# Kernel optimization log

Measured on AMD Instinct MI355X. Metric: run time of the kernel, lower is better.

The kernel has to match this reference:

```python
import jax, jax.numpy as jnp
import numpy as np

ASIZE, VSIZE, HSIZE, MSIZE = 128, 512, 512, 48


def _xavier(key, shape):
    fan_in, fan_out = shape[1], shape[0]
    limit = float(np.sqrt(6.0 / (fan_in + fan_out)))
    return jax.random.uniform(key, shape, jnp.float32, -limit, limit)


def setup_inputs() -> dict:
    key = jax.random.key(0)
    ks = jax.random.split(key, 9)
    B, T = 32, 64
    audio = jax.random.normal(ks[0], (B, T, ASIZE), jnp.float32)
    video = jax.random.normal(ks[1], (B, T, MSIZE, VSIZE), jnp.float32)
    return {
        "audio": audio,
        "video": video,
        "W_audio": _xavier(ks[2], (HSIZE, ASIZE)),
        "b_audio": jnp.zeros((HSIZE,), jnp.float32),
        "W_video": _xavier(ks[3], (HSIZE, VSIZE)),
        "b_video": jnp.zeros((HSIZE,), jnp.float32),
        "W_v": _xavier(ks[4], (MSIZE, HSIZE)),
        "W_g": _xavier(ks[5], (MSIZE, HSIZE)),
        "W_h": _xavier(ks[6], (1, MSIZE)),
    }


def reference(audio, video, W_audio, b_audio, W_video, b_video, W_v, W_g, W_h):
    B, T, N, vsize = video.shape  # N == MSIZE == 48 required by the broadcast
    V = video.reshape(B * T, N, vsize)                      # [BT, N, vsize]
    v = jax.nn.relu(jnp.einsum('bnv,hv->bnh', V, W_video) + b_video)  # [BT,N,h]
    a = jax.nn.relu(audio.reshape(-1, audio.shape[-1]) @ W_audio.T + b_audio)  # [BT,h]
    inter = a @ W_g.T                                        # [BT, m]
    # torch broadcast: [BT,N,m] + [BT,m,1] with N==m -> inter indexed by spatial pos
    content = jnp.einsum('bnh,mh->bnm', v, W_v) + inter[:, :, None]
    z = jnp.einsum('bnm,om->bno', jnp.tanh(content), W_h)[..., 0]  # [BT, N]
    alpha = jax.nn.softmax(z, axis=-1)                        # [BT, N]
    c = jnp.einsum('bn,bnv->bv', alpha, V)                    # [BT, vsize]
    return c.reshape(B, T, vsize)
```

## Files before the change

### kernel.cpp

```cpp
#include <hip/hip_runtime.h>
#include <hip/hip_bf16.h>

typedef __bf16 bf16x8 __attribute__((ext_vector_type(8)));
typedef __bf16 bf16x4 __attribute__((ext_vector_type(4)));
typedef float  f32x4  __attribute__((ext_vector_type(4)));

#define BT    2048
#define MDIM  48

#define WS_WVID  0
#define WS_WV    (512*512*2)
#define WS_WG    (WS_WV + 48*512*2)
#define WS_INTER (WS_WG + 48*512*2)

__global__ __launch_bounds__(256) void convert_weights(
    const float* __restrict__ Wvid, const float* __restrict__ Wv,
    const float* __restrict__ Wg,
    __bf16* __restrict__ wvid_k, __bf16* __restrict__ wv_b,
    __bf16* __restrict__ wg_b) {
    int i = blockIdx.x * blockDim.x + threadIdx.x;
    const int nv = 65536, n2 = 6144;
    if (i < nv) {
        int h = i >> 7, k4 = i & 127;
        float4 f = ((const float4*)Wvid)[i];
        bf16x4 o = {(__bf16)f.x, (__bf16)f.y, (__bf16)f.z, (__bf16)f.w};
        *(bf16x4*)(wvid_k + (size_t)(((k4 >> 1) * 512 + h) * 8 + (k4 & 1) * 4)) = o;
    } else if (i < nv + n2) {
        int j = i - nv;
        float4 f = ((const float4*)Wv)[j];
        bf16x4 o = {(__bf16)f.x, (__bf16)f.y, (__bf16)f.z, (__bf16)f.w};
        ((bf16x4*)wv_b)[j] = o;
    } else {
        int j = i - nv - n2;
        float4 f = ((const float4*)Wg)[j];
        bf16x4 o = {(__bf16)f.x, (__bf16)f.y, (__bf16)f.z, (__bf16)f.w};
        ((bf16x4*)wg_b)[j] = o;
    }
}

__global__ __launch_bounds__(512) void audio_batch(
    const float* __restrict__ audio, const float* __restrict__ Wa,
    const float* __restrict__ ba, const __bf16* __restrict__ wg_b,
    float* __restrict__ inter) {
    __shared__ float  ain[16 * 128];
    __shared__ __bf16 as_s[64 * 17 * 8];

    const int bt0 = blockIdx.x * 16;
    const int t   = threadIdx.x;

    ((float4*)ain)[t] = ((const float4*)(audio + (size_t)bt0 * 128))[t];
    __syncthreads();

    float acc[16];
    float bias = ba[t];
    #pragma unroll
    for (int b = 0; b < 16; ++b) acc[b] = bias;
    const float4* wr = (const float4*)(Wa + (size_t)t * 128);
    #pragma unroll 4
    for (int k4 = 0; k4 < 32; ++k4) {
        float4 wv = wr[k4];
        #pragma unroll
        for (int b = 0; b < 16; ++b) {
            float4 av = ((const float4*)ain)[b * 32 + k4];
            acc[b] += av.x*wv.x + av.y*wv.y + av.z*wv.z + av.w*wv.w;
        }
    }
    #pragma unroll
    for (int b = 0; b < 16; ++b)
        as_s[(((t >> 3) * 17 + b) << 3) | (t & 7)] = (__bf16)fmaxf(acc[b], 0.f);
    __syncthreads();

    const int w = t >> 6, lane = t & 63, l16 = lane & 15, quad = lane >> 4;
    if (w < 3) {
        f32x4 c = {0.f, 0.f, 0.f, 0.f};
        const __bf16* bp = wg_b + (size_t)(w * 16 + l16) * 512 + quad * 8;
        const __bf16* ap = &as_s[((quad * 17 + l16)) * 8];
        bf16x8 aC = *(const bf16x8*)ap;
        bf16x8 bC = *(const bf16x8*)bp;
        #pragma unroll
        for (int kt = 0; kt < 16; ++kt) {
            bf16x8 aN, bN;
            if (kt < 15) {
                aN = *(const bf16x8*)(ap + (kt + 1) * (4 * 17 * 8));
                bN = *(const bf16x8*)(bp + (kt + 1) * 32);
            }
            c = __builtin_amdgcn_mfma_f32_16x16x32_bf16(aC, bC, c, 0, 0, 0);
            if (kt < 15) { aC = aN; bC = bN; }
        }
        #pragma unroll
        for (int r = 0; r < 4; ++r)
            inter[(size_t)(bt0 + quad * 4 + r) * 48 + w * 16 + l16] = c[r];
    }
}

__global__ __launch_bounds__(512, 4) void main_fused(
    const float* __restrict__ video, const float* __restrict__ bvid,
    const __bf16* __restrict__ wvid_k, const __bf16* __restrict__ wv_b,
    const float* __restrict__ Wh, const float* __restrict__ inter_g,
    float* __restrict__ out) {

    __shared__ uint4 pool4[3136];
    __shared__ float inter_s[MDIM];
    __shared__ float z_s[MDIM];
    __shared__ float alpha_s[MDIM];
    __shared__ float content8[256];

    char* pool = (char*)pool4;

    const int bt   = blockIdx.x;
    const int tid  = threadIdx.x;
    const int w    = tid >> 6;
    const int lane = tid & 63;
    const int l16  = lane & 15;
    const int quad = lane >> 4;

    const float* Vg = video + (size_t)bt * (48 * 512);
    const char*  bbase = (const char*)wvid_k;

    if (tid < MDIM) { inter_s[tid] = inter_g[bt * MDIM + tid]; z_s[tid] = 0.f; }
    if (tid < 256) content8[tid] = 0.f;

    const int  s_a    = tid >> 3;
    const int  kcl    = tid & 7;
    const bool stager = (tid < 384);

    if (stager) {
        const float4* p4 = (const float4*)(Vg + s_a * 512 + kcl * 8);
        float4 x = p4[0], y = p4[1];
        bf16x8 g = {(__bf16)x.x, (__bf16)x.y, (__bf16)x.z, (__bf16)x.w,
                    (__bf16)y.x, (__bf16)y.y, (__bf16)y.z, (__bf16)y.w};
        *(bf16x8*)(pool + (kcl * 49 + s_a) * 16) = g;
    }

    const int bIdx0 = quad * 8192 + (w * 64 + l16) * 16;
    bf16x8 bC[4];
    #pragma unroll
    for (int j = 0; j < 4; ++j)
        bC[j] = *(const bf16x8*)(bbase + bIdx0 + j * 256);

    f32x4 acc[3][4];
    #pragma unroll
    for (int mt = 0; mt < 3; ++mt)
        #pragma unroll
        for (int j = 0; j < 4; ++j) {
            f32x4 z = {0.f, 0.f, 0.f, 0.f};
            acc[mt][j] = z;
        }

    __syncthreads();

    #pragma unroll
    for (int c = 0; c < 8; ++c) {
        float4 sx, sy;
        if (c < 7 && stager) {
            const float4* p4 = (const float4*)(Vg + s_a * 512 + ((c + 1) * 8 + kcl) * 8);
            sx = p4[0]; sy = p4[1];
        }
        #pragma unroll
        for (int k = 0; k < 2; ++k) {
            const int kt = c * 2 + k;
            bf16x8 bN[4];
            if (kt < 15) {
                #pragma unroll
                for (int j = 0; j < 4; ++j)
                    bN[j] = *(const bf16x8*)(bbase + bIdx0 + (kt + 1) * 32768 + j * 256);
            }
            bf16x8 a[3];
            #pragma unroll
            for (int mt = 0; mt < 3; ++mt)
                a[mt] = *(const bf16x8*)(pool + ((4 * kt + quad) * 49 + mt * 16 + l16) * 16);
            #pragma unroll
            for (int mt = 0; mt < 3; ++mt)
                #pragma unroll
                for (int j = 0; j < 4; ++j)
                    acc[mt][j] = __builtin_amdgcn_mfma_f32_16x16x32_bf16(
                                     a[mt], bC[j], acc[mt][j], 0, 0, 0);
            if (kt < 15) {
                #pragma unroll
                for (int j = 0; j < 4; ++j) bC[j] = bN[j];
            }
        }
        if (c < 7 && stager) {
            bf16x8 g = {(__bf16)sx.x, (__bf16)sx.y, (__bf16)sx.z, (__bf16)sx.w,
                        (__bf16)sy.x, (__bf16)sy.y, (__bf16)sy.z, (__bf16)sy.w};
            *(bf16x8*)(pool + (((c + 1) * 8 + kcl) * 49 + s_a) * 16) = g;
        }
        __syncthreads();
    }

    #pragma unroll
    for (int j = 0; j < 4; ++j) {
        int h = w * 64 + j * 16 + l16;
        float bias = bvid[h];
        #pragma unroll
        for (int mt = 0; mt < 3; ++mt) {
            #pragma unroll
            for (int r = 0; r < 4; ++r) {
                int s = mt * 16 + quad * 4 + r;
                *(__bf16*)(pool + s * 1040 + h * 2) =
                    (__bf16)fmaxf(acc[mt][j][r] + bias, 0.f);
            }
        }
    }
    __syncthreads();

    {
        int ti = w / 3, tj = w - ti * 3;
        const __bf16* bp = wv_b + (size_t)(tj * 16 + l16) * 512 + quad * 8;
        const char*   ap = pool + (ti * 16 + l16) * 1040 + quad * 16;
        f32x4 c3e = {0.f, 0.f, 0.f, 0.f};
        f32x4 c3o = {0.f, 0.f, 0.f, 0.f};
        #pragma unroll
        for (int kt = 0; kt < 16; kt += 2) {
            bf16x8 a0 = *(const bf16x8*)(ap + kt * 64);
            bf16x8 b0 = *(const bf16x8*)(bp + kt * 32);
            c3e = __builtin_amdgcn_mfma_f32_16x16x32_bf16(a0, b0, c3e, 0, 0, 0);
            bf16x8 a1 = *(const bf16x8*)(ap + (kt + 1) * 64);
            bf16x8 b1 = *(const bf16x8*)(bp + (kt + 1) * 32);
            c3o = __builtin_amdgcn_mfma_f32_16x16x32_bf16(a1, b1, c3o, 0, 0, 0);
        }
        f32x4 c3 = c3e + c3o;
        float wh = Wh[tj * 16 + l16];
        #pragma unroll
        for (int r = 0; r < 4; ++r) {
            int s = ti * 16 + quad * 4 + r;
            float contrib = tanhf(c3[r] + inter_s[s]) * wh;
            contrib += __shfl_xor(contrib, 1);
            contrib += __shfl_xor(contrib, 2);
            contrib += __shfl_xor(contrib, 4);
            contrib += __shfl_xor(contrib, 8);
            if (l16 == 0) atomicAdd(&z_s[s], contrib);
        }
        f32x4 p8 = {0.f, 0.f, 0.f, 0.f};
        #pragma unroll
        for (int q = 0; q < 2; ++q) {
            int kt = 2 * w + q;
            bf16x8 a8 = *(const bf16x8*)(pool + (32 + l16) * 1040 + kt * 64 + quad * 16);
            bf16x8 b8 = *(const bf16x8*)(wv_b + (size_t)(32 + l16) * 512 + kt * 32 + quad * 8);
            p8 = __builtin_amdgcn_mfma_f32_16x16x32_bf16(a8, b8, p8, 0, 0, 0);
        }
        #pragma unroll
        for (int r = 0; r < 4; ++r)
            atomicAdd(&content8[(quad * 4 + r) * 16 + l16], p8[r]);
    }
    __syncthreads();

    if (w == 0) {
        float wh = Wh[32 + l16];
        #pragma unroll
        for (int r = 0; r < 4; ++r) {
            int s = 32 + quad * 4 + r;
            float contrib = tanhf(content8[(quad * 4 + r) * 16 + l16] + inter_s[s]) * wh;
            contrib += __shfl_xor(contrib, 1);
            contrib += __shfl_xor(contrib, 2);
            contrib += __shfl_xor(contrib, 4);
            contrib += __shfl_xor(contrib, 8);
            if (l16 == 0) atomicAdd(&z_s[s], contrib);
        }
    }
    __syncthreads();

    if (w == 0) {
        float x = (lane < MDIM) ? z_s[lane] : -INFINITY;
        float mx = x;
        #pragma unroll
        for (int off = 32; off >= 1; off >>= 1) mx = fmaxf(mx, __shfl_xor(mx, off));
        float e = (lane < MDIM) ? expf(x - mx) : 0.f;
        float sm = e;
        #pragma unroll
        for (int off = 32; off >= 1; off >>= 1) sm += __shfl_xor(sm, off);
        if (lane < MDIM) alpha_s[lane] = e / sm;
    }
    __syncthreads();

    float acc5 = 0.f;
    #pragma unroll
    for (int s = 0; s < MDIM; ++s)
        acc5 += alpha_s[s] * Vg[s * 512 + tid];
    out[(size_t)bt * 512 + tid] = acc5;
}

extern "C" void kernel_launch(void* const* d_in, const int* in_sizes, int n_in,
                              void* d_out, int out_size, void* d_ws, size_t ws_size,
                              hipStream_t stream) {
    const float* audio   = (const float*)d_in[0];
    const float* video   = (const float*)d_in[1];
    const float* W_audio = (const float*)d_in[2];
    const float* b_audio = (const float*)d_in[3];
    const float* W_video = (const float*)d_in[4];
    const float* b_video = (const float*)d_in[5];
    const float* W_v     = (const float*)d_in[6];
    const float* W_g     = (const float*)d_in[7];
    const float* W_h     = (const float*)d_in[8];
    float* out = (float*)d_out;

    char* ws = (char*)d_ws;
    __bf16* wvid_k = (__bf16*)(ws + WS_WVID);
    __bf16* wv_b   = (__bf16*)(ws + WS_WV);
    __bf16* wg_b   = (__bf16*)(ws + WS_WG);
    float*  inter  = (float*)(ws + WS_INTER);

    convert_weights<<<304, 256, 0, stream>>>(W_video, W_v, W_g, wvid_k, wv_b, wg_b);
    audio_batch<<<BT / 16, 512, 0, stream>>>(audio, W_audio, b_audio, wg_b, inter);
    main_fused<<<BT, 512, 0, stream>>>(video, b_video, wvid_k, wv_b, W_h, inter, out);
}
```

Before: 392.4 us.

## Stage video tiles in larger chunks with register prefetch across chunk barriers

The video staging loop now processes four chunks of 128 K-columns instead of eight chunks of 64. Each stager thread loads two spatial rows per chunk. The next chunk's global loads are issued right after the current chunk is written to LDS, so they stay in flight across the whole MFMA block and its barrier. This halves the number of __syncthreads and lengthens the window for hiding global-load latency. The cost is more live registers for the prefetched float4s.

```diff
diff --git a/kernel.cpp b/kernel.cpp
--- a/kernel.cpp
+++ b/kernel.cpp
@@ -120,16 +120,25 @@
     if (tid < MDIM) { inter_s[tid] = inter_g[bt * MDIM + tid]; z_s[tid] = 0.f; }
     if (tid < 256) content8[tid] = 0.f;
 
-    const int  s_a    = tid >> 3;
-    const int  kcl    = tid & 7;
+    const int  s_a0   = tid >> 4;
+    const int  s_a1   = s_a0 + 24;
+    const int  kcl    = tid & 15;
     const bool stager = (tid < 384);
 
+    float4 rx0, ry0, rx1, ry1;
     if (stager) {
-        const float4* p4 = (const float4*)(Vg + s_a * 512 + kcl * 8);
-        float4 x = p4[0], y = p4[1];
-        bf16x8 g = {(__bf16)x.x, (__bf16)x.y, (__bf16)x.z, (__bf16)x.w,
-                    (__bf16)y.x, (__bf16)y.y, (__bf16)y.z, (__bf16)y.w};
-        *(bf16x8*)(pool + (kcl * 49 + s_a) * 16) = g;
+        const float4* p = (const float4*)(Vg + s_a0 * 512 + kcl * 8);
+        const float4* q = (const float4*)(Vg + s_a1 * 512 + kcl * 8);
+        float4 x0 = p[0], y0 = p[1], x1 = q[0], y1 = q[1];
+        bf16x8 g0 = {(__bf16)x0.x, (__bf16)x0.y, (__bf16)x0.z, (__bf16)x0.w,
+                     (__bf16)y0.x, (__bf16)y0.y, (__bf16)y0.z, (__bf16)y0.w};
+        bf16x8 g1 = {(__bf16)x1.x, (__bf16)x1.y, (__bf16)x1.z, (__bf16)x1.w,
+                     (__bf16)y1.x, (__bf16)y1.y, (__bf16)y1.z, (__bf16)y1.w};
+        *(bf16x8*)(pool + (kcl * 49 + s_a0) * 16) = g0;
+        *(bf16x8*)(pool + (kcl * 49 + s_a1) * 16) = g1;
+        const float4* p1 = (const float4*)(Vg + s_a0 * 512 + (16 + kcl) * 8);
+        const float4* q1 = (const float4*)(Vg + s_a1 * 512 + (16 + kcl) * 8);
+        rx0 = p1[0]; ry0 = p1[1]; rx1 = q1[0]; ry1 = q1[1];
     }
 
     const int bIdx0 = quad * 8192 + (w * 64 + l16) * 16;
@@ -150,15 +159,10 @@
     __syncthreads();
 
     #pragma unroll
-    for (int c = 0; c < 8; ++c) {
-        float4 sx, sy;
-        if (c < 7 && stager) {
-            const float4* p4 = (const float4*)(Vg + s_a * 512 + ((c + 1) * 8 + kcl) * 8);
-            sx = p4[0]; sy = p4[1];
-        }
-        #pragma unroll
-        for (int k = 0; k < 2; ++k) {
-            const int kt = c * 2 + k;
+    for (int c = 0; c < 4; ++c) {
+        #pragma unroll
+        for (int k = 0; k < 4; ++k) {
+            const int kt = c * 4 + k;
             bf16x8 bN[4];
             if (kt < 15) {
                 #pragma unroll
@@ -180,10 +184,20 @@
                 for (int j = 0; j < 4; ++j) bC[j] = bN[j];
             }
         }
-        if (c < 7 && stager) {
-            bf16x8 g = {(__bf16)sx.x, (__bf16)sx.y, (__bf16)sx.z, (__bf16)sx.w,
-                        (__bf16)sy.x, (__bf16)sy.y, (__bf16)sy.z, (__bf16)sy.w};
-            *(bf16x8*)(pool + (((c + 1) * 8 + kcl) * 49 + s_a) * 16) = g;
+        if (c < 3 && stager) {
+            const int kc = (c + 1) * 16 + kcl;
+            bf16x8 g0 = {(__bf16)rx0.x, (__bf16)rx0.y, (__bf16)rx0.z, (__bf16)rx0.w,
+                         (__bf16)ry0.x, (__bf16)ry0.y, (__bf16)ry0.z, (__bf16)ry0.w};
+            bf16x8 g1 = {(__bf16)rx1.x, (__bf16)rx1.y, (__bf16)rx1.z, (__bf16)rx1.w,
+                         (__bf16)ry1.x, (__bf16)ry1.y, (__bf16)ry1.z, (__bf16)ry1.w};
+            *(bf16x8*)(pool + (kc * 49 + s_a0) * 16) = g0;
+            *(bf16x8*)(pool + (kc * 49 + s_a1) * 16) = g1;
+            if (c < 2) {
+                const int kc2 = (c + 2) * 16 + kcl;
+                const float4* p = (const float4*)(Vg + s_a0 * 512 + kc2 * 8);
+                const float4* q = (const float4*)(Vg + s_a1 * 512 + kc2 * 8);
+                rx0 = p[0]; ry0 = p[1]; rx1 = q[0]; ry1 = q[1];
+            }
         }
         __syncthreads();
     }
```

Result: slower. 405.2 us (+3.3%).

## Halve main kernel block to 256 threads with wider per-wave N tiles

Applied to the files above, without the earlier changes.

Shrinks the fused per-row block from 512 to 256 threads, giving each wave 128 output columns (8 MFMA N tiles) instead of 64. The video staging now runs in 4 chunks of 16 k-columns loaded by all threads, and the weight register double-buffering is dropped in favour of loading all 8 B fragments per k-step. The attention and output stages are remapped so each thread covers two tiles or two output columns. This halves weight-fragment traffic per block and raises MFMA density per wave, at the cost of more accumulator registers, lower occupancy, and less load/compute overlap.

```diff
diff --git a/kernel.cpp b/kernel.cpp
--- a/kernel.cpp
+++ b/kernel.cpp
@@ -93,7 +93,7 @@
     }
 }
 
-__global__ __launch_bounds__(512, 4) void main_fused(
+__global__ __launch_bounds__(256, 3) void main_fused(
     const float* __restrict__ video, const float* __restrict__ bvid,
     const __bf16* __restrict__ wvid_k, const __bf16* __restrict__ wv_b,
     const float* __restrict__ Wh, const float* __restrict__ inter_g,
@@ -118,31 +118,28 @@
     const char*  bbase = (const char*)wvid_k;
 
     if (tid < MDIM) { inter_s[tid] = inter_g[bt * MDIM + tid]; z_s[tid] = 0.f; }
-    if (tid < 256) content8[tid] = 0.f;
-
-    const int  s_a    = tid >> 3;
-    const int  kcl    = tid & 7;
-    const bool stager = (tid < 384);
-
-    if (stager) {
-        const float4* p4 = (const float4*)(Vg + s_a * 512 + kcl * 8);
-        float4 x = p4[0], y = p4[1];
+    content8[tid] = 0.f;
+
+    const int kcl = tid & 15;
+    const int s_b = tid >> 4;
+
+    #pragma unroll
+    for (int m = 0; m < 3; ++m) {
+        const int s = s_b + m * 16;
+        const float4* p = (const float4*)(Vg + s * 512 + kcl * 8);
+        float4 x = p[0], y = p[1];
         bf16x8 g = {(__bf16)x.x, (__bf16)x.y, (__bf16)x.z, (__bf16)x.w,
                     (__bf16)y.x, (__bf16)y.y, (__bf16)y.z, (__bf16)y.w};
-        *(bf16x8*)(pool + (kcl * 49 + s_a) * 16) = g;
-    }
-
-    const int bIdx0 = quad * 8192 + (w * 64 + l16) * 16;
-    bf16x8 bC[4];
-    #pragma unroll
-    for (int j = 0; j < 4; ++j)
-        bC[j] = *(const bf16x8*)(bbase + bIdx0 + j * 256);
-
-    f32x4 acc[3][4];
+        *(bf16x8*)(pool + (kcl * 49 + s) * 16) = g;
+    }
+
+    const int bIdx0 = quad * 8192 + (w * 128 + l16) * 16;
+
+    f32x4 acc[3][8];
     #pragma unroll
     for (int mt = 0; mt < 3; ++mt)
         #pragma unroll
-        for (int j = 0; j < 4; ++j) {
+        for (int j = 0; j < 8; ++j) {
             f32x4 z = {0.f, 0.f, 0.f, 0.f};
             acc[mt][j] = z;
         }
@@ -150,53 +147,49 @@
     __syncthreads();
 
     #pragma unroll
-    for (int c = 0; c < 8; ++c) {
-        float4 sx, sy;
-        if (c < 7 && stager) {
-            const float4* p4 = (const float4*)(Vg + s_a * 512 + ((c + 1) * 8 + kcl) * 8);
-            sx = p4[0]; sy = p4[1];
-        }
-        #pragma unroll
-        for (int k = 0; k < 2; ++k) {
-            const int kt = c * 2 + k;
-            bf16x8 bN[4];
-            if (kt < 15) {
-                #pragma unroll
-                for (int j = 0; j < 4; ++j)
-                    bN[j] = *(const bf16x8*)(bbase + bIdx0 + (kt + 1) * 32768 + j * 256);
-            }
+    for (int c = 0; c < 4; ++c) {
+        #pragma unroll
+        for (int k = 0; k < 4; ++k) {
+            const int kt = c * 4 + k;
             bf16x8 a[3];
             #pragma unroll
             for (int mt = 0; mt < 3; ++mt)
                 a[mt] = *(const bf16x8*)(pool + ((4 * kt + quad) * 49 + mt * 16 + l16) * 16);
+            bf16x8 b[8];
+            #pragma unroll
+            for (int j = 0; j < 8; ++j)
+                b[j] = *(const bf16x8*)(bbase + bIdx0 + kt * 32768 + j * 256);
             #pragma unroll
             for (int mt = 0; mt < 3; ++mt)
                 #pragma unroll
-                for (int j = 0; j < 4; ++j)
+                for (int j = 0; j < 8; ++j)
                     acc[mt][j] = __builtin_amdgcn_mfma_f32_16x16x32_bf16(
-                                     a[mt], bC[j], acc[mt][j], 0, 0, 0);
-            if (kt < 15) {
-                #pragma unroll
-                for (int j = 0; j < 4; ++j) bC[j] = bN[j];
-            }
-        }
-        if (c < 7 && stager) {
-            bf16x8 g = {(__bf16)sx.x, (__bf16)sx.y, (__bf16)sx.z, (__bf16)sx.w,
-                        (__bf16)sy.x, (__bf16)sy.y, (__bf16)sy.z, (__bf16)sy.w};
-            *(bf16x8*)(pool + (((c + 1) * 8 + kcl) * 49 + s_a) * 16) = g;
+                                     a[mt], b[j], acc[mt][j], 0, 0, 0);
+        }
+        if (c < 3) {
+            #pragma unroll
+            for (int m = 0; m < 3; ++m) {
+                const int s  = s_b + m * 16;
+                const int kc = (c + 1) * 16 + kcl;
+                const float4* p = (const float4*)(Vg + s * 512 + kc * 8);
+                float4 x = p[0], y = p[1];
+                bf16x8 g = {(__bf16)x.x, (__bf16)x.y, (__bf16)x.z, (__bf16)x.w,
+                            (__bf16)y.x, (__bf16)y.y, (__bf16)y.z, (__bf16)y.w};
+                *(bf16x8*)(pool + (kc * 49 + s) * 16) = g;
+            }
         }
         __syncthreads();
     }
 
     #pragma unroll
-    for (int j = 0; j < 4; ++j) {
-        int h = w * 64 + j * 16 + l16;
+    for (int j = 0; j < 8; ++j) {
+        const int h = w * 128 + j * 16 + l16;
         float bias = bvid[h];
         #pragma unroll
         for (int mt = 0; mt < 3; ++mt) {
             #pragma unroll
             for (int r = 0; r < 4; ++r) {
-                int s = mt * 16 + quad * 4 + r;
+                const int s = mt * 16 + quad * 4 + r;
                 *(__bf16*)(pool + s * 1040 + h * 2) =
                     (__bf16)fmaxf(acc[mt][j][r] + bias, 0.f);
             }
@@ -205,36 +198,40 @@
     __syncthreads();
 
     {
-        int ti = w / 3, tj = w - ti * 3;
-        const __bf16* bp = wv_b + (size_t)(tj * 16 + l16) * 512 + quad * 8;
-        const char*   ap = pool + (ti * 16 + l16) * 1040 + quad * 16;
-        f32x4 c3e = {0.f, 0.f, 0.f, 0.f};
-        f32x4 c3o = {0.f, 0.f, 0.f, 0.f};
-        #pragma unroll
-        for (int kt = 0; kt < 16; kt += 2) {
-            bf16x8 a0 = *(const bf16x8*)(ap + kt * 64);
-            bf16x8 b0 = *(const bf16x8*)(bp + kt * 32);
-            c3e = __builtin_amdgcn_mfma_f32_16x16x32_bf16(a0, b0, c3e, 0, 0, 0);
-            bf16x8 a1 = *(const bf16x8*)(ap + (kt + 1) * 64);
-            bf16x8 b1 = *(const bf16x8*)(bp + (kt + 1) * 32);
-            c3o = __builtin_amdgcn_mfma_f32_16x16x32_bf16(a1, b1, c3o, 0, 0, 0);
-        }
-        f32x4 c3 = c3e + c3o;
-        float wh = Wh[tj * 16 + l16];
-        #pragma unroll
-        for (int r = 0; r < 4; ++r) {
-            int s = ti * 16 + quad * 4 + r;
-            float contrib = tanhf(c3[r] + inter_s[s]) * wh;
-            contrib += __shfl_xor(contrib, 1);
-            contrib += __shfl_xor(contrib, 2);
-            contrib += __shfl_xor(contrib, 4);
-            contrib += __shfl_xor(contrib, 8);
-            if (l16 == 0) atomicAdd(&z_s[s], contrib);
+        #pragma unroll
+        for (int half = 0; half < 2; ++half) {
+            const int T  = w + half * 4;
+            const int ti = T / 3, tj = T - ti * 3;
+            const __bf16* bp = wv_b + (size_t)(tj * 16 + l16) * 512 + quad * 8;
+            const char*   ap = pool + (ti * 16 + l16) * 1040 + quad * 16;
+            f32x4 c3e = {0.f, 0.f, 0.f, 0.f};
+            f32x4 c3o = {0.f, 0.f, 0.f, 0.f};
+            #pragma unroll
+            for (int kt = 0; kt < 16; kt += 2) {
+                bf16x8 a0 = *(const bf16x8*)(ap + kt * 64);
+                bf16x8 b0 = *(const bf16x8*)(bp + kt * 32);
+                c3e = __builtin_amdgcn_mfma_f32_16x16x32_bf16(a0, b0, c3e, 0, 0, 0);
+                bf16x8 a1 = *(const bf16x8*)(ap + (kt + 1) * 64);
+                bf16x8 b1 = *(const bf16x8*)(bp + (kt + 1) * 32);
+                c3o = __builtin_amdgcn_mfma_f32_16x16x32_bf16(a1, b1, c3o, 0, 0, 0);
+            }
+            f32x4 c3 = c3e + c3o;
+            float wh = Wh[tj * 16 + l16];
+            #pragma unroll
+            for (int r = 0; r < 4; ++r) {
+                const int s = ti * 16 + quad * 4 + r;
+                float contrib = tanhf(c3[r] + inter_s[s]) * wh;
+                contrib += __shfl_xor(contrib, 1);
+                contrib += __shfl_xor(contrib, 2);
+                contrib += __shfl_xor(contrib, 4);
+                contrib += __shfl_xor(contrib, 8);
+                if (l16 == 0) atomicAdd(&z_s[s], contrib);
+            }
         }
         f32x4 p8 = {0.f, 0.f, 0.f, 0.f};
         #pragma unroll
-        for (int q = 0; q < 2; ++q) {
-            int kt = 2 * w + q;
+        for (int q = 0; q < 4; ++q) {
+            const int kt = 4 * w + q;
             bf16x8 a8 = *(const bf16x8*)(pool + (32 + l16) * 1040 + kt * 64 + quad * 16);
             bf16x8 b8 = *(const bf16x8*)(wv_b + (size_t)(32 + l16) * 512 + kt * 32 + quad * 8);
             p8 = __builtin_amdgcn_mfma_f32_16x16x32_bf16(a8, b8, p8, 0, 0, 0);
@@ -249,7 +246,7 @@
         float wh = Wh[32 + l16];
         #pragma unroll
         for (int r = 0; r < 4; ++r) {
-            int s = 32 + quad * 4 + r;
+            const int s = 32 + quad * 4 + r;
             float contrib = tanhf(content8[(quad * 4 + r) * 16 + l16] + inter_s[s]) * wh;
             contrib += __shfl_xor(contrib, 1);
             contrib += __shfl_xor(contrib, 2);
@@ -273,11 +270,15 @@
     }
     __syncthreads();
 
-    float acc5 = 0.f;
-    #pragma unroll
-    for (int s = 0; s < MDIM; ++s)
-        acc5 += alpha_s[s] * Vg[s * 512 + tid];
-    out[(size_t)bt * 512 + tid] = acc5;
+    float a5 = 0.f, b5 = 0.f;
+    #pragma unroll
+    for (int s = 0; s < MDIM; ++s) {
+        const float al = alpha_s[s];
+        a5 += al * Vg[s * 512 + tid];
+        b5 += al * Vg[s * 512 + 256 + tid];
+    }
+    out[(size_t)bt * 512 + tid]       = a5;
+    out[(size_t)bt * 512 + 256 + tid] = b5;
 }
 
 extern "C" void kernel_launch(void* const* d_in, const int* in_sizes, int n_in,
@@ -302,5 +303,5 @@
 
     convert_weights<<<304, 256, 0, stream>>>(W_video, W_v, W_g, wvid_k, wv_b, wg_b);
     audio_batch<<<BT / 16, 512, 0, stream>>>(audio, W_audio, b_audio, wg_b, inter);
-    main_fused<<<BT, 512, 0, stream>>>(video, b_video, wvid_k, wv_b, W_h, inter, out);
+    main_fused<<<BT, 256, 0, stream>>>(video, b_video, wvid_k, wv_b, W_h, inter, out);
 }
```

New measurement: 432.2 us. 10.2% more time.
